# Optimization experiments

Measured on AMD Instinct MI355X. Metric: run time of the kernel, lower is better.

Reference implementation:

```python
import jax, jax.numpy as jnp
import numpy as np

B, C, H, W = 4, 256, 64, 64
INTER = C // 2
BN_EPS = 1e-5


def setup_inputs() -> dict:
    key = jax.random.key(0)
    ks = jax.random.split(key, 12)
    s = 0.05
    return {
        "x": jax.random.normal(ks[0], (B, C, H, W), dtype=jnp.float32),
        "theta_w": jax.random.normal(ks[1], (INTER, C), dtype=jnp.float32) * s,
        "theta_b": jax.random.normal(ks[2], (INTER,), dtype=jnp.float32) * s,
        "phi_w": jax.random.normal(ks[3], (INTER, C), dtype=jnp.float32) * s,
        "phi_b": jax.random.normal(ks[4], (INTER,), dtype=jnp.float32) * s,
        "g_w": jax.random.normal(ks[5], (INTER, C), dtype=jnp.float32) * s,
        "g_b": jax.random.normal(ks[6], (INTER,), dtype=jnp.float32) * s,
        "W_w": jax.random.normal(ks[7], (C, INTER), dtype=jnp.float32) * s,
        "W_b": jax.random.normal(ks[8], (C,), dtype=jnp.float32) * s,
        "bn_gamma": jnp.ones((C,), dtype=jnp.float32),
        "bn_beta": jnp.zeros((C,), dtype=jnp.float32),
    }


def _conv1x1(x, w, b):
    # 1x1 conv == per-pixel GEMM: (B,C,H,W) x (O,C) -> (B,O,H,W)
    return jnp.einsum("bchw,oc->bohw", x, w) + b[None, :, None, None]


def reference(x, theta_w, theta_b, phi_w, phi_b, g_w, g_b, W_w, W_b, bn_gamma, bn_beta):
    b, c, h, w = x.shape
    hw = h * w
    theta = _conv1x1(x, theta_w, theta_b).reshape(b, -1, hw)  # (B, inter, HW) -> queries
    phi = _conv1x1(x, phi_w, phi_b).reshape(b, -1, hw)        # (B, inter, HW) -> keys
    g = _conv1x1(x, g_w, g_b).reshape(b, -1, hw)              # (B, inter, HW) -> values
    # f[n,m] = <theta[:,n], phi[:,m]> over all HW spatial positions
    f = jnp.einsum("bin,bim->bnm", theta, phi)                # (B, HW, HW)
    attn = jax.nn.softmax(f, axis=-1)
    y = jnp.einsum("bnm,bim->bin", attn, g)                   # (B, inter, HW)
    y = y.reshape(b, c // 2, h, w)
    wy = _conv1x1(y, W_w, W_b)                                # (B, C, H, W)
    # BatchNorm2d (training-mode batch statistics, per channel)
    mean = jnp.mean(wy, axis=(0, 2, 3), keepdims=True)
    var = jnp.var(wy, axis=(0, 2, 3), keepdims=True)
    wy_bn = bn_gamma[None, :, None, None] * (wy - mean) * jax.lax.rsqrt(var + BN_EPS) + bn_beta[None, :, None, None]
    return wy_bn + x
```

## Files before the change

### kernel.cpp

```cpp
#include <hip/hip_runtime.h>
#include <hip/hip_bf16.h>

#define HWN   4096
#define CIN   256
#define NINTER 128
#define NBATCH 4
#define BN_EPS 1e-5f
#define LOG2E 1.4426950408889634f
#define SMAX  64.0f

typedef __bf16 bf16_t;
typedef __bf16 bf16x8 __attribute__((ext_vector_type(8)));
typedef __bf16 bf16x4 __attribute__((ext_vector_type(4)));
typedef float  f32x4  __attribute__((ext_vector_type(4)));
typedef float  f32x16 __attribute__((ext_vector_type(16)));

__device__ __forceinline__ float fexp2(float x) {
  return __builtin_amdgcn_exp2f(x);
}

__device__ __forceinline__ void split_bf16(float v, bf16_t& h, bf16_t& l) {
  h = (bf16_t)v;
  l = (bf16_t)(v - (float)h);
}

__global__ __launch_bounds__(256) void convert_weights(
    const float* __restrict__ tw, const float* __restrict__ pw,
    const float* __restrict__ gw, const float* __restrict__ ww,
    bf16_t* __restrict__ out) {
  int i = blockIdx.x * 256 + threadIdx.x;
  float v;
  if (i < 32768)        v = tw[i];
  else if (i < 65536)   v = pw[i - 32768];
  else if (i < 98304)   v = gw[i - 65536];
  else                  v = ww[i - 98304];
  bf16_t h, l;
  split_bf16(v, h, l);
  out[i] = h;
  out[131072 + i] = l;
}

__global__ __launch_bounds__(256, 4) void qkv_kernel(
    const float* __restrict__ x, const bf16_t* __restrict__ wbf,
    const float* __restrict__ tb, const float* __restrict__ pb,
    const float* __restrict__ gb,
    bf16_t* __restrict__ Qh, bf16_t* __restrict__ Kh, bf16_t* __restrict__ V) {
  const int ntb  = blockIdx.x;
  const int b    = blockIdx.y;
  const int tid  = threadIdx.x;
  const int lane = tid & 63;
  const int wv   = tid >> 6;
  const int l31  = lane & 31;
  const int half = lane >> 5;

  __shared__ __align__(16) bf16_t smem[4608];
  bf16_t (*xTh)[72] = (bf16_t(*)[72])smem;
  bf16_t (*xTl)[72] = (bf16_t(*)[72])(smem + 2304);
  bf16_t (*Tr)[136] = (bf16_t(*)[136])smem;

  const bf16_t* Th = wbf;
  const bf16_t* Tl = wbf + 131072;
  const bf16_t* Ph = wbf + 32768;
  const bf16_t* Pl = wbf + 131072 + 32768;
  const bf16_t* Gh = wbf + 65536;
  const float*  xb = x + (size_t)b * CIN * HWN + ntb * 32;

  f32x16 aq, ak, av;
#pragma unroll
  for (int i = 0; i < 16; i++) { aq[i] = 0.f; ak[i] = 0.f; av[i] = 0.f; }

  for (int c0 = 0; c0 < 256; c0 += 64) {
    __syncthreads();
#pragma unroll
    for (int i = 0; i < 8; i++) {
      int idx = tid + i * 256;
      int cc = idx >> 5;
      int nn = idx & 31;
      float v = xb[(size_t)(c0 + cc) * HWN + nn];
      bf16_t h, l;
      split_bf16(v, h, l);
      xTh[nn][cc] = h;
      xTl[nn][cc] = l;
    }
    __syncthreads();
#pragma unroll
    for (int kk = 0; kk < 64; kk += 16) {
      size_t woff = (size_t)(32 * wv + l31) * 256 + c0 + kk + half * 8;
      bf16x8 th = *(const bf16x8*)(Th + woff);
      bf16x8 tl = *(const bf16x8*)(Tl + woff);
      bf16x8 ph = *(const bf16x8*)(Ph + woff);
      bf16x8 pl = *(const bf16x8*)(Pl + woff);
      bf16x8 gh = *(const bf16x8*)(Gh + woff);
      bf16x8 bh = *(const bf16x8*)(&xTh[l31][kk + half * 8]);
      bf16x8 bl = *(const bf16x8*)(&xTl[l31][kk + half * 8]);
      aq = __builtin_amdgcn_mfma_f32_32x32x16_bf16(th, bh, aq, 0, 0, 0);
      aq = __builtin_amdgcn_mfma_f32_32x32x16_bf16(th, bl, aq, 0, 0, 0);
      aq = __builtin_amdgcn_mfma_f32_32x32x16_bf16(tl, bh, aq, 0, 0, 0);
      ak = __builtin_amdgcn_mfma_f32_32x32x16_bf16(ph, bh, ak, 0, 0, 0);
      ak = __builtin_amdgcn_mfma_f32_32x32x16_bf16(ph, bl, ak, 0, 0, 0);
      ak = __builtin_amdgcn_mfma_f32_32x32x16_bf16(pl, bh, ak, 0, 0, 0);
      av = __builtin_amdgcn_mfma_f32_32x32x16_bf16(gh, bh, av, 0, 0, 0);
    }
  }

  const int trow = tid >> 3;
  const int tc16 = (tid & 7) * 16;
  bf16_t* qh = Qh + ((size_t)b * HWN + ntb * 32) * NINTER;
  bf16_t* kh = Kh + ((size_t)b * HWN + ntb * 32) * NINTER;

#pragma unroll
  for (int rnd = 0; rnd < 2; rnd++) {
    __syncthreads();
#pragma unroll
    for (int rg = 0; rg < 4; rg++) {
      int och0 = 32 * wv + 8 * rg + 4 * half;
#pragma unroll
      for (int j = 0; j < 4; j++) {
        float v = (rnd == 0) ? (aq[rg * 4 + j] + tb[och0 + j]) * LOG2E
                             : (ak[rg * 4 + j] + pb[och0 + j]);
        Tr[l31][och0 + j] = (bf16_t)v;
      }
    }
    __syncthreads();
    bf16_t* dst = (rnd == 0) ? qh : kh;
    bf16x8 v0 = *(const bf16x8*)(&Tr[trow][tc16]);
    bf16x8 v1 = *(const bf16x8*)(&Tr[trow][tc16 + 8]);
    *(bf16x8*)(dst + (size_t)trow * NINTER + tc16) = v0;
    *(bf16x8*)(dst + (size_t)trow * NINTER + tc16 + 8) = v1;
  }

  const int n = ntb * 32 + l31;
  bf16_t* vd = V + (size_t)b * NINTER * HWN;
#pragma unroll
  for (int r = 0; r < 16; r++) {
    int och = 32 * wv + (r & 3) + 8 * (r >> 2) + 4 * half;
    vd[(size_t)och * HWN + n] = (bf16_t)(av[r] + gb[och]);
  }
}

template<int NCv>
__global__ __launch_bounds__(512, 1) void attn_kernel(
    const bf16_t* __restrict__ Qh, const bf16_t* __restrict__ Kh,
    const bf16_t* __restrict__ V,
    float* __restrict__ Opart, float* __restrict__ Lp) {
  constexpr int CH = HWN / NCv;
  constexpr int NT = CH / 32;
  const int qt    = blockIdx.x;
  const int chunk = blockIdx.y;
  const int b     = blockIdx.z;
  const int tid   = threadIdx.x;
  const int lane  = tid & 63;
  const int wv    = tid >> 6;
  const int l15   = lane & 15;
  const int quad  = lane >> 4;
  const int kbase = chunk * CH;

  __shared__ __align__(16) bf16_t Klds[32][136];
  __shared__ __align__(16) bf16_t Vlds[144][56];
  __shared__ __align__(16) bf16_t Plds[8][32][40];

  const bf16_t* Qhb = Qh + (size_t)b * HWN * NINTER;
  const bf16_t* Khb = Kh + (size_t)b * HWN * NINTER;
  const bf16_t* Vb  = V + (size_t)b * NINTER * HWN;

  if (tid < 112) {
    int row = 128 + tid / 7;
    int c8 = (tid % 7) * 8;
    bf16x8 v;
#pragma unroll
    for (int j = 0; j < 8; j++) v[j] = (bf16_t)((row == 128) ? 1.0f : 0.0f);
    *(bf16x8*)(&Vlds[row][c8]) = v;
  }

  bf16x8 qf[2][4];
#pragma unroll
  for (int qs = 0; qs < 2; qs++) {
    const int qrow = qt * 256 + wv * 32 + qs * 16 + l15;
#pragma unroll
    for (int kc = 0; kc < 4; kc++)
      qf[qs][kc] = *(const bf16x8*)(Qhb + (size_t)qrow * NINTER + kc * 32 + quad * 8);
  }

  f32x4 o[2][8], ol[2];
#pragma unroll
  for (int qs = 0; qs < 2; qs++) {
#pragma unroll
    for (int dt = 0; dt < 8; dt++)
#pragma unroll
      for (int i = 0; i < 4; i++) o[qs][dt][i] = 0.f;
#pragma unroll
    for (int i = 0; i < 4; i++) ol[qs][i] = 0.f;
  }

  const int krow = tid >> 4;
  const int kc8  = (tid & 15) * 8;
  const int vrow = tid >> 2;
  const int vc8  = (tid & 3) * 8;
  const bf16_t* kgp = Khb + (size_t)(kbase + krow) * NINTER + kc8;
  const bf16_t* vgp = Vb + (size_t)vrow * HWN + kbase + vc8;

  uint4 ka = *(const uint4*)(kgp);
  uint4 va = *(const uint4*)(vgp);

  for (int t = 0; t < NT; t++) {
    __syncthreads();
    *(uint4*)(&Klds[krow][kc8]) = ka;
    *(uint4*)(&Vlds[vrow][vc8]) = va;
    __syncthreads();

    if (t + 1 < NT) {
      ka = *(const uint4*)(kgp + (size_t)(t + 1) * 32 * NINTER);
      va = *(const uint4*)(vgp + (t + 1) * 32);
    }

    f32x4 s[2][2];
#pragma unroll
    for (int qs = 0; qs < 2; qs++)
#pragma unroll
      for (int ks = 0; ks < 2; ks++)
#pragma unroll
        for (int i = 0; i < 4; i++) s[qs][ks][i] = 0.f;
#pragma unroll
    for (int ks = 0; ks < 2; ks++)
#pragma unroll
      for (int kc = 0; kc < 4; kc++) {
        bf16x8 kf = *(const bf16x8*)(&Klds[ks * 16 + l15][kc * 32 + quad * 8]);
        s[0][ks] = __builtin_amdgcn_mfma_f32_16x16x32_bf16(kf, qf[0][kc], s[0][ks], 0, 0, 0);
        s[1][ks] = __builtin_amdgcn_mfma_f32_16x16x32_bf16(kf, qf[1][kc], s[1][ks], 0, 0, 0);
      }

#pragma unroll
    for (int qs = 0; qs < 2; qs++)
#pragma unroll
      for (int ks = 0; ks < 2; ks++) {
        bf16x4 p4;
#pragma unroll
        for (int r = 0; r < 4; r++)
          p4[r] = (bf16_t)fexp2(s[qs][ks][r] - SMAX);
        *(bf16x4*)(&Plds[wv][qs * 16 + l15][ks * 16 + quad * 4]) = p4;
      }

    bf16x8 pf0 = *(const bf16x8*)(&Plds[wv][l15][quad * 8]);
    bf16x8 pf1 = *(const bf16x8*)(&Plds[wv][16 + l15][quad * 8]);
#pragma unroll
    for (int dt = 0; dt < 8; dt++) {
      bf16x8 vf = *(const bf16x8*)(&Vlds[dt * 16 + l15][quad * 8]);
      o[0][dt] = __builtin_amdgcn_mfma_f32_16x16x32_bf16(pf0, vf, o[0][dt], 0, 0, 0);
      o[1][dt] = __builtin_amdgcn_mfma_f32_16x16x32_bf16(pf1, vf, o[1][dt], 0, 0, 0);
    }
    bf16x8 vfl = *(const bf16x8*)(&Vlds[128 + l15][quad * 8]);
    ol[0] = __builtin_amdgcn_mfma_f32_16x16x32_bf16(pf0, vfl, ol[0], 0, 0, 0);
    ol[1] = __builtin_amdgcn_mfma_f32_16x16x32_bf16(pf1, vfl, ol[1], 0, 0, 0);
  }

  float* Ob = Opart + ((size_t)(b * NCv + chunk) * HWN) * NINTER;
#pragma unroll
  for (int qs = 0; qs < 2; qs++)
#pragma unroll
    for (int r = 0; r < 4; r++) {
      int n = qt * 256 + wv * 32 + qs * 16 + quad * 4 + r;
#pragma unroll
      for (int dt = 0; dt < 8; dt++)
        Ob[(size_t)n * NINTER + dt * 16 + l15] = o[qs][dt][r];
      if (l15 == 0)
        Lp[(size_t)(b * NCv + chunk) * HWN + n] = ol[qs][r];
    }
}

template<int NCv>
__global__ __launch_bounds__(256, 4) void wconv_kernel(
    const bf16_t* __restrict__ Wbf, const float* __restrict__ Opart,
    const float* __restrict__ Lp, const float* __restrict__ Wb,
    bf16_t* __restrict__ WY) {
  const int ntb = blockIdx.x;
  const int b   = blockIdx.y;
  const int tid = threadIdx.x;
  const int lane = tid & 63;
  const int wv   = tid >> 6;
  const int l31  = lane & 31;
  const int half = lane >> 5;

  __shared__ __align__(16) bf16_t Ylds[32][136];
  __shared__ float Linv[32];

  if (tid < 32) {
    int n = ntb * 32 + tid;
    float ls = 0.f;
#pragma unroll
    for (int c = 0; c < NCv; c++) ls += Lp[(size_t)(b * NCv + c) * HWN + n];
    Linv[tid] = 1.f / ls;
  }

  const int nrow = tid >> 3;
  const int dgrp = tid & 7;
  float oacc[16];
#pragma unroll
  for (int j = 0; j < 16; j++) oacc[j] = 0.f;
#pragma unroll
  for (int c = 0; c < NCv; c++) {
    const float* Op = Opart +
        ((size_t)(b * NCv + c) * HWN + ntb * 32 + nrow) * NINTER + dgrp * 16;
#pragma unroll
    for (int q = 0; q < 4; q++) {
      f32x4 v = *(const f32x4*)(Op + q * 4);
#pragma unroll
      for (int j = 0; j < 4; j++) oacc[q * 4 + j] += v[j];
    }
  }
  __syncthreads();
  {
    float inv = Linv[nrow];
    bf16x8 y0, y1;
#pragma unroll
    for (int j = 0; j < 8; j++) {
      y0[j] = (bf16_t)(oacc[j] * inv);
      y1[j] = (bf16_t)(oacc[8 + j] * inv);
    }
    *(bf16x8*)(&Ylds[nrow][dgrp * 16]) = y0;
    *(bf16x8*)(&Ylds[nrow][dgrp * 16 + 8]) = y1;
  }
  __syncthreads();

  const bf16_t* Wh = Wbf + 98304;
  f32x16 acc[2];
#pragma unroll
  for (int c = 0; c < 2; c++)
#pragma unroll
    for (int i = 0; i < 16; i++) acc[c][i] = 0.f;

#pragma unroll
  for (int k0 = 0; k0 < 128; k0 += 16) {
    bf16x8 a0 = *(const bf16x8*)(Wh + (size_t)(wv * 64 + l31) * NINTER + k0 + half * 8);
    bf16x8 a1 = *(const bf16x8*)(Wh + (size_t)(wv * 64 + 32 + l31) * NINTER + k0 + half * 8);
    bf16x8 b0 = *(const bf16x8*)(&Ylds[l31][k0 + half * 8]);
    acc[0] = __builtin_amdgcn_mfma_f32_32x32x16_bf16(a0, b0, acc[0], 0, 0, 0);
    acc[1] = __builtin_amdgcn_mfma_f32_32x32x16_bf16(a1, b0, acc[1], 0, 0, 0);
  }

  bf16_t* dst = WY + (size_t)b * 256 * HWN + ntb * 32;
#pragma unroll
  for (int ct = 0; ct < 2; ct++)
#pragma unroll
    for (int r = 0; r < 16; r++) {
      int co = wv * 64 + ct * 32 + (r & 3) + 8 * (r >> 2) + 4 * half;
      dst[(size_t)co * HWN + l31] = (bf16_t)(acc[ct][r] + Wb[co]);
    }
}

__global__ __launch_bounds__(256) void stats_kernel(
    const bf16_t* __restrict__ WY, float* __restrict__ stats) {
  const int c = blockIdx.x;
  const int tid = threadIdx.x;
  float s = 0.f, s2 = 0.f;
  for (int b = 0; b < NBATCH; b++) {
    const bf16_t* p = WY + ((size_t)b * 256 + c) * HWN;
    for (int i = tid * 8; i < HWN; i += 2048) {
      bf16x8 v8 = *(const bf16x8*)(p + i);
#pragma unroll
      for (int j = 0; j < 8; j++) {
        float v = (float)v8[j];
        s += v;
        s2 += v * v;
      }
    }
  }
#pragma unroll
  for (int off = 1; off < 64; off <<= 1) {
    s += __shfl_xor(s, off);
    s2 += __shfl_xor(s2, off);
  }
  __shared__ float red[8];
  int wv = tid >> 6;
  if ((tid & 63) == 0) { red[wv] = s; red[4 + wv] = s2; }
  __syncthreads();
  if (tid == 0) {
    float S = red[0] + red[1] + red[2] + red[3];
    float S2 = red[4] + red[5] + red[6] + red[7];
    float mean = S * (1.f / 16384.f);
    float var = S2 * (1.f / 16384.f) - mean * mean;
    stats[c] = mean;
    stats[256 + c] = rsqrtf(var + BN_EPS);
  }
}

__global__ __launch_bounds__(256) void bn_kernel(
    const bf16_t* __restrict__ WY, const float* __restrict__ x,
    const float* __restrict__ stats, const float* __restrict__ gamma,
    const float* __restrict__ beta, float* __restrict__ out) {
  int idx = blockIdx.x * 256 + threadIdx.x;
  int e = idx * 4;
  int c = (e >> 12) & 255;
  bf16x4 w4 = *(const bf16x4*)(WY + e);
  float4 xv = *(const float4*)(x + e);
  float mean = stats[c];
  float g = gamma[c] * stats[256 + c];
  float bb = beta[c];
  float4 o;
  o.x = g * ((float)w4[0] - mean) + bb + xv.x;
  o.y = g * ((float)w4[1] - mean) + bb + xv.y;
  o.z = g * ((float)w4[2] - mean) + bb + xv.z;
  o.w = g * ((float)w4[3] - mean) + bb + xv.w;
  *(float4*)(out + e) = o;
}

extern "C" void kernel_launch(void* const* d_in, const int* in_sizes, int n_in,
                              void* d_out, int out_size, void* d_ws, size_t ws_size,
                              hipStream_t stream) {
  const float* x       = (const float*)d_in[0];
  const float* theta_b = (const float*)d_in[2];
  const float* phi_b   = (const float*)d_in[4];
  const float* g_b     = (const float*)d_in[6];
  const float* W_b     = (const float*)d_in[8];
  const float* bn_g    = (const float*)d_in[9];
  const float* bn_b    = (const float*)d_in[10];
  float* out = (float*)d_out;

  constexpr int NC = 4;
  const size_t opb = (size_t)NC * HWN * NINTER * NBATCH * 4;
  const size_t lpb = (size_t)NC * HWN * NBATCH * 4;

  char* ws = (char*)d_ws;
  bf16_t* Qh  = (bf16_t*)(ws);
  bf16_t* Kh  = (bf16_t*)(ws + 4194304);
  bf16_t* V   = (bf16_t*)(ws + 8388608);
  float*  OP  = (float*)(ws + 12582912);
  bf16_t* WY  = (bf16_t*)(ws + 12582912 + opb);
  float*  LP  = (float*)(ws + 12582912 + opb + 8388608);
  bf16_t* WBF = (bf16_t*)(ws + 12582912 + opb + 8388608 + lpb);
  float*  ST  = (float*)(ws + 12582912 + opb + 8388608 + lpb + 524288);

  convert_weights<<<512, 256, 0, stream>>>(
      (const float*)d_in[1], (const float*)d_in[3],
      (const float*)d_in[5], (const float*)d_in[7], WBF);
  qkv_kernel<<<dim3(128, NBATCH), 256, 0, stream>>>(
      x, WBF, theta_b, phi_b, g_b, Qh, Kh, V);
  attn_kernel<NC><<<dim3(16, NC, NBATCH), 512, 0, stream>>>(
      Qh, Kh, V, OP, LP);
  wconv_kernel<NC><<<dim3(128, NBATCH), 256, 0, stream>>>(
      WBF, OP, LP, W_b, WY);
  stats_kernel<<<256, 256, 0, stream>>>(WY, ST);
  bn_kernel<<<4096, 256, 0, stream>>>(WY, x, ST, bn_g, bn_b, out);
}
```

Baseline: 175.9 us.

## Fuse weight bf16 conversion into consumers and double attention key tile to 64

Drops the separate convert_weights launch. qkv and wconv now read fp32 weights directly and split them to bf16 hi/lo in registers, removing one kernel launch and a workspace round-trip. The attention kernel now processes 64 keys per iteration instead of 32, halving loop iterations and barriers at the cost of larger LDS tiles and more registers. Converting weights redundantly in every block adds ALU work and doubles weight load bytes, and occupancy hints were lowered from 4 to 2.

```diff
diff --git a/kernel.cpp b/kernel.cpp
--- a/kernel.cpp
+++ b/kernel.cpp
@@ -13,6 +13,7 @@
 typedef __bf16 bf16x8 __attribute__((ext_vector_type(8)));
 typedef __bf16 bf16x4 __attribute__((ext_vector_type(4)));
 typedef float  f32x4  __attribute__((ext_vector_type(4)));
+typedef float  f32x8  __attribute__((ext_vector_type(8)));
 typedef float  f32x16 __attribute__((ext_vector_type(16)));
 
 __device__ __forceinline__ float fexp2(float x) {
@@ -24,24 +25,9 @@
   l = (bf16_t)(v - (float)h);
 }
 
-__global__ __launch_bounds__(256) void convert_weights(
-    const float* __restrict__ tw, const float* __restrict__ pw,
-    const float* __restrict__ gw, const float* __restrict__ ww,
-    bf16_t* __restrict__ out) {
-  int i = blockIdx.x * 256 + threadIdx.x;
-  float v;
-  if (i < 32768)        v = tw[i];
-  else if (i < 65536)   v = pw[i - 32768];
-  else if (i < 98304)   v = gw[i - 65536];
-  else                  v = ww[i - 98304];
-  bf16_t h, l;
-  split_bf16(v, h, l);
-  out[i] = h;
-  out[131072 + i] = l;
-}
-
-__global__ __launch_bounds__(256, 4) void qkv_kernel(
-    const float* __restrict__ x, const bf16_t* __restrict__ wbf,
+__global__ __launch_bounds__(256, 2) void qkv_kernel(
+    const float* __restrict__ x, const float* __restrict__ tw,
+    const float* __restrict__ pw, const float* __restrict__ gw,
     const float* __restrict__ tb, const float* __restrict__ pb,
     const float* __restrict__ gb,
     bf16_t* __restrict__ Qh, bf16_t* __restrict__ Kh, bf16_t* __restrict__ V) {
@@ -58,12 +44,7 @@
   bf16_t (*xTl)[72] = (bf16_t(*)[72])(smem + 2304);
   bf16_t (*Tr)[136] = (bf16_t(*)[136])smem;
 
-  const bf16_t* Th = wbf;
-  const bf16_t* Tl = wbf + 131072;
-  const bf16_t* Ph = wbf + 32768;
-  const bf16_t* Pl = wbf + 131072 + 32768;
-  const bf16_t* Gh = wbf + 65536;
-  const float*  xb = x + (size_t)b * CIN * HWN + ntb * 32;
+  const float* xb = x + (size_t)b * CIN * HWN + ntb * 32;
 
   f32x16 aq, ak, av;
 #pragma unroll
@@ -86,11 +67,17 @@
 #pragma unroll
     for (int kk = 0; kk < 64; kk += 16) {
       size_t woff = (size_t)(32 * wv + l31) * 256 + c0 + kk + half * 8;
-      bf16x8 th = *(const bf16x8*)(Th + woff);
-      bf16x8 tl = *(const bf16x8*)(Tl + woff);
-      bf16x8 ph = *(const bf16x8*)(Ph + woff);
-      bf16x8 pl = *(const bf16x8*)(Pl + woff);
-      bf16x8 gh = *(const bf16x8*)(Gh + woff);
+      f32x8 tw8 = *(const f32x8*)(tw + woff);
+      f32x8 pw8 = *(const f32x8*)(pw + woff);
+      f32x8 gw8 = *(const f32x8*)(gw + woff);
+      bf16x8 th, tl, ph, pl, gh;
+#pragma unroll
+      for (int j = 0; j < 8; j++) {
+        bf16_t h, l;
+        split_bf16(tw8[j], h, l); th[j] = h; tl[j] = l;
+        split_bf16(pw8[j], h, l); ph[j] = h; pl[j] = l;
+        gh[j] = (bf16_t)gw8[j];
+      }
       bf16x8 bh = *(const bf16x8*)(&xTh[l31][kk + half * 8]);
       bf16x8 bl = *(const bf16x8*)(&xTl[l31][kk + half * 8]);
       aq = __builtin_amdgcn_mfma_f32_32x32x16_bf16(th, bh, aq, 0, 0, 0);
@@ -144,7 +131,7 @@
     const bf16_t* __restrict__ V,
     float* __restrict__ Opart, float* __restrict__ Lp) {
   constexpr int CH = HWN / NCv;
-  constexpr int NT = CH / 32;
+  constexpr int NT = CH / 64;
   const int qt    = blockIdx.x;
   const int chunk = blockIdx.y;
   const int b     = blockIdx.z;
@@ -155,17 +142,17 @@
   const int quad  = lane >> 4;
   const int kbase = chunk * CH;
 
-  __shared__ __align__(16) bf16_t Klds[32][136];
-  __shared__ __align__(16) bf16_t Vlds[144][56];
-  __shared__ __align__(16) bf16_t Plds[8][32][40];
+  __shared__ __align__(16) bf16_t Klds[64][136];
+  __shared__ __align__(16) bf16_t Vlds[144][72];
+  __shared__ __align__(16) bf16_t Plds[8][32][72];
 
   const bf16_t* Qhb = Qh + (size_t)b * HWN * NINTER;
   const bf16_t* Khb = Kh + (size_t)b * HWN * NINTER;
   const bf16_t* Vb  = V + (size_t)b * NINTER * HWN;
 
-  if (tid < 112) {
-    int row = 128 + tid / 7;
-    int c8 = (tid % 7) * 8;
+  if (tid < 144) {
+    int row = 128 + tid / 9;
+    int c8 = (tid % 9) * 8;
     bf16x8 v;
 #pragma unroll
     for (int j = 0; j < 8; j++) v[j] = (bf16_t)((row == 128) ? 1.0f : 0.0f);
@@ -194,34 +181,42 @@
 
   const int krow = tid >> 4;
   const int kc8  = (tid & 15) * 8;
-  const int vrow = tid >> 2;
-  const int vc8  = (tid & 3) * 8;
+  const int vrow = tid >> 3;
+  const int vc8  = (tid & 7) * 8;
   const bf16_t* kgp = Khb + (size_t)(kbase + krow) * NINTER + kc8;
   const bf16_t* vgp = Vb + (size_t)vrow * HWN + kbase + vc8;
 
   uint4 ka = *(const uint4*)(kgp);
+  uint4 kb = *(const uint4*)(kgp + (size_t)32 * NINTER);
   uint4 va = *(const uint4*)(vgp);
+  uint4 vb = *(const uint4*)(vgp + (size_t)64 * HWN);
 
   for (int t = 0; t < NT; t++) {
     __syncthreads();
     *(uint4*)(&Klds[krow][kc8]) = ka;
+    *(uint4*)(&Klds[krow + 32][kc8]) = kb;
     *(uint4*)(&Vlds[vrow][vc8]) = va;
+    *(uint4*)(&Vlds[vrow + 64][vc8]) = vb;
     __syncthreads();
 
     if (t + 1 < NT) {
-      ka = *(const uint4*)(kgp + (size_t)(t + 1) * 32 * NINTER);
-      va = *(const uint4*)(vgp + (t + 1) * 32);
-    }
-
-    f32x4 s[2][2];
+      const bf16_t* kn = kgp + (size_t)(t + 1) * 64 * NINTER;
+      const bf16_t* vn = vgp + (t + 1) * 64;
+      ka = *(const uint4*)(kn);
+      kb = *(const uint4*)(kn + (size_t)32 * NINTER);
+      va = *(const uint4*)(vn);
+      vb = *(const uint4*)(vn + (size_t)64 * HWN);
+    }
+
+    f32x4 s[2][4];
 #pragma unroll
     for (int qs = 0; qs < 2; qs++)
 #pragma unroll
-      for (int ks = 0; ks < 2; ks++)
+      for (int ks = 0; ks < 4; ks++)
 #pragma unroll
         for (int i = 0; i < 4; i++) s[qs][ks][i] = 0.f;
 #pragma unroll
-    for (int ks = 0; ks < 2; ks++)
+    for (int ks = 0; ks < 4; ks++)
 #pragma unroll
       for (int kc = 0; kc < 4; kc++) {
         bf16x8 kf = *(const bf16x8*)(&Klds[ks * 16 + l15][kc * 32 + quad * 8]);
@@ -232,7 +227,7 @@
 #pragma unroll
     for (int qs = 0; qs < 2; qs++)
 #pragma unroll
-      for (int ks = 0; ks < 2; ks++) {
+      for (int ks = 0; ks < 4; ks++) {
         bf16x4 p4;
 #pragma unroll
         for (int r = 0; r < 4; r++)
@@ -240,17 +235,20 @@
         *(bf16x4*)(&Plds[wv][qs * 16 + l15][ks * 16 + quad * 4]) = p4;
       }
 
-    bf16x8 pf0 = *(const bf16x8*)(&Plds[wv][l15][quad * 8]);
-    bf16x8 pf1 = *(const bf16x8*)(&Plds[wv][16 + l15][quad * 8]);
-#pragma unroll
-    for (int dt = 0; dt < 8; dt++) {
-      bf16x8 vf = *(const bf16x8*)(&Vlds[dt * 16 + l15][quad * 8]);
-      o[0][dt] = __builtin_amdgcn_mfma_f32_16x16x32_bf16(pf0, vf, o[0][dt], 0, 0, 0);
-      o[1][dt] = __builtin_amdgcn_mfma_f32_16x16x32_bf16(pf1, vf, o[1][dt], 0, 0, 0);
-    }
-    bf16x8 vfl = *(const bf16x8*)(&Vlds[128 + l15][quad * 8]);
-    ol[0] = __builtin_amdgcn_mfma_f32_16x16x32_bf16(pf0, vfl, ol[0], 0, 0, 0);
-    ol[1] = __builtin_amdgcn_mfma_f32_16x16x32_bf16(pf1, vfl, ol[1], 0, 0, 0);
+#pragma unroll
+    for (int kh = 0; kh < 2; kh++) {
+      bf16x8 pf0 = *(const bf16x8*)(&Plds[wv][l15][kh * 32 + quad * 8]);
+      bf16x8 pf1 = *(const bf16x8*)(&Plds[wv][16 + l15][kh * 32 + quad * 8]);
+#pragma unroll
+      for (int dt = 0; dt < 8; dt++) {
+        bf16x8 vf = *(const bf16x8*)(&Vlds[dt * 16 + l15][kh * 32 + quad * 8]);
+        o[0][dt] = __builtin_amdgcn_mfma_f32_16x16x32_bf16(pf0, vf, o[0][dt], 0, 0, 0);
+        o[1][dt] = __builtin_amdgcn_mfma_f32_16x16x32_bf16(pf1, vf, o[1][dt], 0, 0, 0);
+      }
+      bf16x8 vfl = *(const bf16x8*)(&Vlds[128 + l15][kh * 32 + quad * 8]);
+      ol[0] = __builtin_amdgcn_mfma_f32_16x16x32_bf16(pf0, vfl, ol[0], 0, 0, 0);
+      ol[1] = __builtin_amdgcn_mfma_f32_16x16x32_bf16(pf1, vfl, ol[1], 0, 0, 0);
+    }
   }
 
   float* Ob = Opart + ((size_t)(b * NCv + chunk) * HWN) * NINTER;
@@ -268,8 +266,8 @@
 }
 
 template<int NCv>
-__global__ __launch_bounds__(256, 4) void wconv_kernel(
-    const bf16_t* __restrict__ Wbf, const float* __restrict__ Opart,
+__global__ __launch_bounds__(256, 2) void wconv_kernel(
+    const float* __restrict__ Ww, const float* __restrict__ Opart,
     const float* __restrict__ Lp, const float* __restrict__ Wb,
     bf16_t* __restrict__ WY) {
   const int ntb = blockIdx.x;
@@ -321,7 +319,6 @@
   }
   __syncthreads();
 
-  const bf16_t* Wh = Wbf + 98304;
   f32x16 acc[2];
 #pragma unroll
   for (int c = 0; c < 2; c++)
@@ -330,8 +327,14 @@
 
 #pragma unroll
   for (int k0 = 0; k0 < 128; k0 += 16) {
-    bf16x8 a0 = *(const bf16x8*)(Wh + (size_t)(wv * 64 + l31) * NINTER + k0 + half * 8);
-    bf16x8 a1 = *(const bf16x8*)(Wh + (size_t)(wv * 64 + 32 + l31) * NINTER + k0 + half * 8);
+    f32x8 w0 = *(const f32x8*)(Ww + (size_t)(wv * 64 + l31) * NINTER + k0 + half * 8);
+    f32x8 w1 = *(const f32x8*)(Ww + (size_t)(wv * 64 + 32 + l31) * NINTER + k0 + half * 8);
+    bf16x8 a0, a1;
+#pragma unroll
+    for (int j = 0; j < 8; j++) {
+      a0[j] = (bf16_t)w0[j];
+      a1[j] = (bf16_t)w1[j];
+    }
     bf16x8 b0 = *(const bf16x8*)(&Ylds[l31][k0 + half * 8]);
     acc[0] = __builtin_amdgcn_mfma_f32_32x32x16_bf16(a0, b0, acc[0], 0, 0, 0);
     acc[1] = __builtin_amdgcn_mfma_f32_32x32x16_bf16(a1, b0, acc[1], 0, 0, 0);
@@ -407,9 +410,13 @@
                               void* d_out, int out_size, void* d_ws, size_t ws_size,
                               hipStream_t stream) {
   const float* x       = (const float*)d_in[0];
+  const float* theta_w = (const float*)d_in[1];
   const float* theta_b = (const float*)d_in[2];
+  const float* phi_w   = (const float*)d_in[3];
   const float* phi_b   = (const float*)d_in[4];
+  const float* g_w     = (const float*)d_in[5];
   const float* g_b     = (const float*)d_in[6];
+  const float* W_w     = (const float*)d_in[7];
   const float* W_b     = (const float*)d_in[8];
   const float* bn_g    = (const float*)d_in[9];
   const float* bn_b    = (const float*)d_in[10];
@@ -426,18 +433,14 @@
   float*  OP  = (float*)(ws + 12582912);
   bf16_t* WY  = (bf16_t*)(ws + 12582912 + opb);
   float*  LP  = (float*)(ws + 12582912 + opb + 8388608);
-  bf16_t* WBF = (bf16_t*)(ws + 12582912 + opb + 8388608 + lpb);
   float*  ST  = (float*)(ws + 12582912 + opb + 8388608 + lpb + 524288);
 
-  convert_weights<<<512, 256, 0, stream>>>(
-      (const float*)d_in[1], (const float*)d_in[3],
-      (const float*)d_in[5], (const float*)d_in[7], WBF);
   qkv_kernel<<<dim3(128, NBATCH), 256, 0, stream>>>(
-      x, WBF, theta_b, phi_b, g_b, Qh, Kh, V);
+      x, theta_w, phi_w, g_w, theta_b, phi_b, g_b, Qh, Kh, V);
   attn_kernel<NC><<<dim3(16, NC, NBATCH), 512, 0, stream>>>(
       Qh, Kh, V, OP, LP);
   wconv_kernel<NC><<<dim3(128, NBATCH), 256, 0, stream>>>(
-      WBF, OP, LP, W_b, WY);
+      W_w, OP, LP, W_b, WY);
   stats_kernel<<<256, 256, 0, stream>>>(WY, ST);
   bn_kernel<<<4096, 256, 0, stream>>>(WY, x, ST, bn_g, bn_b, out);
 }
```

After: 178.4 us. No clear change (+1.4%).

## Double attention key tile to 64, allow two blocks per CU, split keys eightfold

Applied to the files above, without the earlier changes.

The attention kernel now processes 64 keys per loop step instead of 32, staging twice as much K and V in shared memory per barrier pair. Launch bounds allow two 512-thread blocks per CU. When the workspace is large enough, the key dimension is split into 8 chunks instead of 4, which doubles the grid size. The aim is fewer barriers, more MFMA work per LDS stage, and better occupancy. The cost is more LDS and register pressure, and larger partial-output buffers for the wconv reduction to read.

```diff
diff --git a/kernel.cpp b/kernel.cpp
--- a/kernel.cpp
+++ b/kernel.cpp
@@ -139,12 +139,12 @@
 }
 
 template<int NCv>
-__global__ __launch_bounds__(512, 1) void attn_kernel(
+__global__ __launch_bounds__(512, 2) void attn_kernel(
     const bf16_t* __restrict__ Qh, const bf16_t* __restrict__ Kh,
     const bf16_t* __restrict__ V,
     float* __restrict__ Opart, float* __restrict__ Lp) {
   constexpr int CH = HWN / NCv;
-  constexpr int NT = CH / 32;
+  constexpr int NT = CH / 64;
   const int qt    = blockIdx.x;
   const int chunk = blockIdx.y;
   const int b     = blockIdx.z;
@@ -155,17 +155,17 @@
   const int quad  = lane >> 4;
   const int kbase = chunk * CH;
 
-  __shared__ __align__(16) bf16_t Klds[32][136];
-  __shared__ __align__(16) bf16_t Vlds[144][56];
-  __shared__ __align__(16) bf16_t Plds[8][32][40];
+  __shared__ __align__(16) bf16_t Klds[64][136];
+  __shared__ __align__(16) bf16_t Vlds[144][72];
+  __shared__ __align__(16) bf16_t Plds[8][32][72];
 
   const bf16_t* Qhb = Qh + (size_t)b * HWN * NINTER;
   const bf16_t* Khb = Kh + (size_t)b * HWN * NINTER;
   const bf16_t* Vb  = V + (size_t)b * NINTER * HWN;
 
-  if (tid < 112) {
-    int row = 128 + tid / 7;
-    int c8 = (tid % 7) * 8;
+  if (tid < 144) {
+    int row = 128 + tid / 9;
+    int c8 = (tid % 9) * 8;
     bf16x8 v;
 #pragma unroll
     for (int j = 0; j < 8; j++) v[j] = (bf16_t)((row == 128) ? 1.0f : 0.0f);
@@ -194,34 +194,42 @@
 
   const int krow = tid >> 4;
   const int kc8  = (tid & 15) * 8;
-  const int vrow = tid >> 2;
-  const int vc8  = (tid & 3) * 8;
+  const int vrow = tid >> 3;
+  const int vc8  = (tid & 7) * 8;
   const bf16_t* kgp = Khb + (size_t)(kbase + krow) * NINTER + kc8;
   const bf16_t* vgp = Vb + (size_t)vrow * HWN + kbase + vc8;
 
   uint4 ka = *(const uint4*)(kgp);
+  uint4 kb = *(const uint4*)(kgp + (size_t)32 * NINTER);
   uint4 va = *(const uint4*)(vgp);
+  uint4 vb = *(const uint4*)(vgp + (size_t)64 * HWN);
 
   for (int t = 0; t < NT; t++) {
     __syncthreads();
     *(uint4*)(&Klds[krow][kc8]) = ka;
+    *(uint4*)(&Klds[krow + 32][kc8]) = kb;
     *(uint4*)(&Vlds[vrow][vc8]) = va;
+    *(uint4*)(&Vlds[vrow + 64][vc8]) = vb;
     __syncthreads();
 
     if (t + 1 < NT) {
-      ka = *(const uint4*)(kgp + (size_t)(t + 1) * 32 * NINTER);
-      va = *(const uint4*)(vgp + (t + 1) * 32);
-    }
-
-    f32x4 s[2][2];
+      const bf16_t* kn = kgp + (size_t)(t + 1) * 64 * NINTER;
+      const bf16_t* vn = vgp + (t + 1) * 64;
+      ka = *(const uint4*)(kn);
+      kb = *(const uint4*)(kn + (size_t)32 * NINTER);
+      va = *(const uint4*)(vn);
+      vb = *(const uint4*)(vn + (size_t)64 * HWN);
+    }
+
+    f32x4 s[2][4];
 #pragma unroll
     for (int qs = 0; qs < 2; qs++)
 #pragma unroll
-      for (int ks = 0; ks < 2; ks++)
+      for (int ks = 0; ks < 4; ks++)
 #pragma unroll
         for (int i = 0; i < 4; i++) s[qs][ks][i] = 0.f;
 #pragma unroll
-    for (int ks = 0; ks < 2; ks++)
+    for (int ks = 0; ks < 4; ks++)
 #pragma unroll
       for (int kc = 0; kc < 4; kc++) {
         bf16x8 kf = *(const bf16x8*)(&Klds[ks * 16 + l15][kc * 32 + quad * 8]);
@@ -232,7 +240,7 @@
 #pragma unroll
     for (int qs = 0; qs < 2; qs++)
 #pragma unroll
-      for (int ks = 0; ks < 2; ks++) {
+      for (int ks = 0; ks < 4; ks++) {
         bf16x4 p4;
 #pragma unroll
         for (int r = 0; r < 4; r++)
@@ -240,17 +248,20 @@
         *(bf16x4*)(&Plds[wv][qs * 16 + l15][ks * 16 + quad * 4]) = p4;
       }
 
-    bf16x8 pf0 = *(const bf16x8*)(&Plds[wv][l15][quad * 8]);
-    bf16x8 pf1 = *(const bf16x8*)(&Plds[wv][16 + l15][quad * 8]);
-#pragma unroll
-    for (int dt = 0; dt < 8; dt++) {
-      bf16x8 vf = *(const bf16x8*)(&Vlds[dt * 16 + l15][quad * 8]);
-      o[0][dt] = __builtin_amdgcn_mfma_f32_16x16x32_bf16(pf0, vf, o[0][dt], 0, 0, 0);
-      o[1][dt] = __builtin_amdgcn_mfma_f32_16x16x32_bf16(pf1, vf, o[1][dt], 0, 0, 0);
-    }
-    bf16x8 vfl = *(const bf16x8*)(&Vlds[128 + l15][quad * 8]);
-    ol[0] = __builtin_amdgcn_mfma_f32_16x16x32_bf16(pf0, vfl, ol[0], 0, 0, 0);
-    ol[1] = __builtin_amdgcn_mfma_f32_16x16x32_bf16(pf1, vfl, ol[1], 0, 0, 0);
+#pragma unroll
+    for (int kh = 0; kh < 2; kh++) {
+      bf16x8 pf0 = *(const bf16x8*)(&Plds[wv][l15][kh * 32 + quad * 8]);
+      bf16x8 pf1 = *(const bf16x8*)(&Plds[wv][16 + l15][kh * 32 + quad * 8]);
+#pragma unroll
+      for (int dt = 0; dt < 8; dt++) {
+        bf16x8 vf = *(const bf16x8*)(&Vlds[dt * 16 + l15][kh * 32 + quad * 8]);
+        o[0][dt] = __builtin_amdgcn_mfma_f32_16x16x32_bf16(pf0, vf, o[0][dt], 0, 0, 0);
+        o[1][dt] = __builtin_amdgcn_mfma_f32_16x16x32_bf16(pf1, vf, o[1][dt], 0, 0, 0);
+      }
+      bf16x8 vfl = *(const bf16x8*)(&Vlds[128 + l15][kh * 32 + quad * 8]);
+      ol[0] = __builtin_amdgcn_mfma_f32_16x16x32_bf16(pf0, vfl, ol[0], 0, 0, 0);
+      ol[1] = __builtin_amdgcn_mfma_f32_16x16x32_bf16(pf1, vfl, ol[1], 0, 0, 0);
+    }
   }
 
   float* Ob = Opart + ((size_t)(b * NCv + chunk) * HWN) * NINTER;
@@ -415,9 +426,11 @@
   const float* bn_b    = (const float*)d_in[10];
   float* out = (float*)d_out;
 
-  constexpr int NC = 4;
-  const size_t opb = (size_t)NC * HWN * NINTER * NBATCH * 4;
-  const size_t lpb = (size_t)NC * HWN * NBATCH * 4;
+  const size_t NEED8 = 12582912ull + 67108864ull + 8388608ull + 524288ull +
+                       524288ull + 2048ull;
+  const int nc = (ws_size >= NEED8) ? 8 : 4;
+  const size_t opb = (size_t)nc * HWN * NINTER * NBATCH * 4;
+  const size_t lpb = (size_t)nc * HWN * NBATCH * 4;
 
   char* ws = (char*)d_ws;
   bf16_t* Qh  = (bf16_t*)(ws);
@@ -434,10 +447,13 @@
       (const float*)d_in[5], (const float*)d_in[7], WBF);
   qkv_kernel<<<dim3(128, NBATCH), 256, 0, stream>>>(
       x, WBF, theta_b, phi_b, g_b, Qh, Kh, V);
-  attn_kernel<NC><<<dim3(16, NC, NBATCH), 512, 0, stream>>>(
-      Qh, Kh, V, OP, LP);
-  wconv_kernel<NC><<<dim3(128, NBATCH), 256, 0, stream>>>(
-      WBF, OP, LP, W_b, WY);
+  if (nc == 8) {
+    attn_kernel<8><<<dim3(16, 8, NBATCH), 512, 0, stream>>>(Qh, Kh, V, OP, LP);
+    wconv_kernel<8><<<dim3(128, NBATCH), 256, 0, stream>>>(WBF, OP, LP, W_b, WY);
+  } else {
+    attn_kernel<4><<<dim3(16, 4, NBATCH), 512, 0, stream>>>(Qh, Kh, V, OP, LP);
+    wconv_kernel<4><<<dim3(128, NBATCH), 256, 0, stream>>>(WBF, OP, LP, W_b, WY);
+  }
   stats_kernel<<<256, 256, 0, stream>>>(WY, ST);
   bn_kernel<<<4096, 256, 0, stream>>>(WY, x, ST, bn_g, bn_b, out);
 }
```

New measurement: 192.5 us. +9.4%, slower.
